# Performance work log

Measured on AMD Instinct MI355X. Metric: run time of the kernel, lower is better.

The kernel has to match this reference:

```python
import jax, jax.numpy as jnp
from jax import lax
import numpy as np

D_MODEL = 2048
NUM_EXPERTS = 16
NUM_TOKENS = 8192  # must be divisible by NUM_EXPERTS (balanced assignment)


def setup_inputs() -> dict:
    key = jax.random.key(0)
    k1, k2 = jax.random.split(key)
    features = jax.random.normal(k1, (NUM_TOKENS, D_MODEL), dtype=jnp.float32)
    # gate weight (orthogonal init in torch; gaussian is fine for a numerical baseline)
    W = jax.random.normal(k2, (NUM_EXPERTS, D_MODEL), dtype=jnp.float32) * 0.1
    b = jnp.zeros((NUM_EXPERTS,), dtype=jnp.float32)
    return {"features": features, "W": W, "b": b, "is_training": 1}


def _balanced_assignment(scores):
    """Greedy balanced assignment: each expert receives exactly T//E tokens.
    Deterministic stand-in for the cpp auction-based balanced_assignment: scan
    over tokens, each token takes its best-scoring expert with remaining capacity.
    Returns sort_by_expert: token indices sorted (stably) by assigned expert."""
    T, E = scores.shape
    cap_per_expert = T // E

    def step(cap, s):  # cap: [E] remaining capacity, s: [E] token's scores
        masked = jnp.where(cap > 0, s, -jnp.inf)
        e = jnp.argmax(masked)
        return cap.at[e].add(-1), e

    _, tok2exp = lax.scan(step, jnp.full((E,), cap_per_expert, dtype=jnp.int32), scores)
    sort_by_expert = jnp.argsort(tok2exp, stable=True)  # [T] token ids grouped by expert
    return sort_by_expert


def reference(features, W, b, is_training):
    # gating computed under no_grad in the original
    affinities = lax.stop_gradient(features @ W.T + b)  # [T, E]
    T, E = affinities.shape
    cap = T // E

    sort_by_expert = _balanced_assignment(affinities)

    routing_probs = jax.nn.softmax(affinities, axis=1)  # [T, E]

    # gather_scores: permute probs into expert order, pick each token's score for
    # its assigned expert, then un-permute back to original token order.
    sorted_probs = routing_probs[sort_by_expert]                 # [T, E]
    expert_idx = (jnp.arange(T) // cap)[:, None]                 # [T, 1], balanced splits
    gathered = jnp.take_along_axis(sorted_probs, expert_idx, axis=1)  # [T, 1]
    i_sort = jnp.argsort(sort_by_expert)                         # inverse permutation
    gathered_scores = gathered[i_sort]                           # [T, 1]

    return sort_by_expert, gathered_scores
```

## Files before the change

### kernel.cpp

```cpp
#include <hip/hip_runtime.h>
#include <hip/hip_bf16.h>
#include <math.h>

#define T_TOK 8192
#define D_MODEL 2048
#define N_EXP 16
#define CAP 512
#define NSEG (T_TOK / 64)


__device__ __forceinline__ unsigned int f2ord(float f) {
    unsigned int b = __float_as_uint(f);
    return (b & 0x80000000u) ? ~b : (b | 0x80000000u);
}

__global__ __launch_bounds__(512, 4) void gemm_finalize_kernel(
    const float* __restrict__ feat, const float* __restrict__ W,
    const float* __restrict__ bias,
    unsigned long long* __restrict__ pref, float* __restrict__ probs)
{
    __shared__ float flds[8][D_MODEL];
    __shared__ float afft[8][N_EXP];

    const int tid  = threadIdx.x;
    const int wave = tid >> 6, lane = tid & 63;
    const int tbase = blockIdx.x * 8;

    {
        const float4* src = (const float4*)(feat + (size_t)tbase * D_MODEL);
        float4* dst = (float4*)&flds[0][0];
        #pragma unroll
        for (int i = 0; i < 8; ++i)
            dst[tid + i * 512] = src[tid + i * 512];
    }

    const float* w0 = W + (size_t)(wave * 2) * D_MODEL + lane * 4;
    const float* w1 = w0 + D_MODEL;

    float acc[16];
    #pragma unroll
    for (int i = 0; i < 16; ++i) acc[i] = 0.f;

    float4 wv0 = *(const float4*)(w0);
    float4 wv1 = *(const float4*)(w1);
    __syncthreads();

    #pragma unroll
    for (int j = 0; j < 8; ++j) {
        float4 wn0, wn1;
        if (j < 7) {
            wn0 = *(const float4*)(w0 + (j + 1) * 256);
            wn1 = *(const float4*)(w1 + (j + 1) * 256);
        } else {
            wn0 = wv0; wn1 = wv1;
        }
        const float* fl = &flds[0][0] + j * 256 + lane * 4;
        #pragma unroll
        for (int r = 0; r < 8; ++r) {
            float4 f = *(const float4*)(fl + r * D_MODEL);
            acc[r * 2 + 0] += f.x * wv0.x;
            acc[r * 2 + 0] += f.y * wv0.y;
            acc[r * 2 + 0] += f.z * wv0.z;
            acc[r * 2 + 0] += f.w * wv0.w;
            acc[r * 2 + 1] += f.x * wv1.x;
            acc[r * 2 + 1] += f.y * wv1.y;
            acc[r * 2 + 1] += f.z * wv1.z;
            acc[r * 2 + 1] += f.w * wv1.w;
        }
        wv0 = wn0; wv1 = wn1;
    }

    #pragma unroll
    for (int step = 0; step < 4; ++step) {
        const int m    = 1 << step;
        const int half = 8 >> step;
        const bool hi  = (lane & m) != 0;
        #pragma unroll
        for (int jj = 0; jj < half; ++jj) {
            float send = hi ? acc[jj] : acc[jj + half];
            float recv = __shfl_xor(send, m, 64);
            acc[jj] = (hi ? acc[jj + half] : acc[jj]) + recv;
        }
    }
    acc[0] += __shfl_xor(acc[0], 16, 64);
    acc[0] += __shfl_xor(acc[0], 32, 64);

    if (lane < 16) {
        const int slot = ((lane & 1) << 3) | (((lane >> 1) & 1) << 2)
                       | (((lane >> 2) & 1) << 1) | ((lane >> 3) & 1);
        const int r = slot >> 1, el = slot & 1;
        afft[r][wave * 2 + el] = acc[0];
    }
    __syncthreads();

    const int tk = tbase + wave;
    const int j  = lane & 15;
    float v = afft[wave][j] + bias[j];

    float mx = v;
    #pragma unroll
    for (int d = 1; d < 16; d <<= 1)
        mx = fmaxf(mx, __shfl_xor(mx, d, 16));

    float ex = __expf(v - mx);

    float s = 0.f;
    #pragma unroll
    for (int e2 = 0; e2 < N_EXP; ++e2)
        s += __shfl(ex, e2, 16);

    if (lane < 16)
        probs[(size_t)tk * N_EXP + lane] = ex / s;

    unsigned long long key = ((unsigned long long)f2ord(v) << 4)
                           | (unsigned long long)(15 - j);
    int rank = 0;
    #pragma unroll
    for (int d = 1; d < 16; ++d) {
        unsigned long long o = __shfl_xor(key, d, 16);
        rank += (o > key) ? 1 : 0;
    }
    unsigned long long contrib = ((unsigned long long)j) << (4 * (15 - rank));
    #pragma unroll
    for (int d = 1; d < 16; d <<= 1)
        contrib |= __shfl_xor(contrib, d, 16);
    if (lane == 0)
        pref[tk] = contrib;
}

__global__ __launch_bounds__(512, 1) void events_kernel(
    const unsigned long long* __restrict__ pref, int* __restrict__ evt,
    int* __restrict__ gsync)
{
    __shared__ unsigned long long segmask[N_EXP][NSEG];
    __shared__ int fparr[N_EXP];

    const int tid  = threadIdx.x;
    const int wave = tid >> 6, lane = tid & 63;
    const unsigned long long lt_mask = (1ull << lane) - 1ull;

    if (tid == 0) *gsync = 0;

    unsigned long long myPref[16];
    #pragma unroll
    for (int k = 0; k < 16; ++k) myPref[k] = pref[tid + 512 * k];

    #pragma unroll
    for (int k = 0; k < 16; ++k) {
        const int s = k * 8 + wave;
        const int c = (int)(myPref[k] >> 60);
        #pragma unroll
        for (int e = 0; e < N_EXP; ++e) {
            unsigned long long mm = __ballot(c == e);
            if (lane == e) segmask[e][s] = mm;
        }
    }
    __syncthreads();

    const int eA = wave, eB = wave + 8;
    int capA = CAP, capB = CAP;
    unsigned long long m0A = 0, m1A = 0, m0B = 0, m1B = 0;
    int excl0A = 0, excl1A = 0, excl0B = 0, excl1B = 0;
    int segF = 0;
    unsigned long long mlep = 0;
    unsigned int avail = 0xFFFFu;
    int myp = 0, myf = 0;

    for (int round = 0; round < N_EXP; ++round) {
        {
            int exf = (segF < 64) ? __shfl(excl0A, segF, 64) : __shfl(excl1A, segF - 64, 64);
            unsigned long long mf = (segF < 64) ? __shfl(m0A, segF, 64) : __shfl(m1A, segF - 64, 64);
            capA -= exf + (int)__popcll(mf & mlep);
            exf = (segF < 64) ? __shfl(excl0B, segF, 64) : __shfl(excl1B, segF - 64, 64);
            mf  = (segF < 64) ? __shfl(m0B, segF, 64) : __shfl(m1B, segF - 64, 64);
            capB -= exf + (int)__popcll(mf & mlep);
        }

        unsigned long long a0 = segmask[eA][lane];
        unsigned long long a1 = segmask[eA][64 + lane];
        unsigned long long b0 = segmask[eB][lane];
        unsigned long long b1 = segmask[eB][64 + lane];
        if (lane < segF)            { a0 = 0; b0 = 0; }
        else if (lane == segF)      { a0 &= ~mlep; b0 &= ~mlep; }
        if (64 + lane < segF)       { a1 = 0; b1 = 0; }
        else if (64 + lane == segF) { a1 &= ~mlep; b1 &= ~mlep; }
        m0A = a0; m1A = a1; m0B = b0; m1B = b1;

        const int c0A = (int)__popcll(a0), c1A = (int)__popcll(a1);
        const int c0B = (int)__popcll(b0), c1B = (int)__popcll(b1);
        int v0A = c0A, v1A = c1A, v0B = c0B, v1B = c1B;
        #pragma unroll
        for (int d = 1; d < 64; d <<= 1) {
            int t0 = __shfl_up(v0A, d, 64);
            int t1 = __shfl_up(v1A, d, 64);
            int t2 = __shfl_up(v0B, d, 64);
            int t3 = __shfl_up(v1B, d, 64);
            if (lane >= d) { v0A += t0; v1A += t1; v0B += t2; v1B += t3; }
        }
        const int tot0A = __shfl(v0A, 63, 64);
        const int tot0B = __shfl(v0B, 63, 64);
        excl0A = v0A - c0A;
        excl1A = tot0A + v1A - c1A;
        excl0B = v0B - c0B;
        excl1B = tot0B + v1B - c1B;

        int fpA = 0x7FFFFFFF;
        if ((avail >> eA) & 1u) {
            const int need = capA;
            int segc = -1, kk = 0;
            if (excl0A < need && excl0A + c0A >= need)      { segc = lane;      kk = need - excl0A; }
            else if (excl1A < need && excl1A + c1A >= need) { segc = 64 + lane; kk = need - excl1A; }
            unsigned long long bb = __ballot(segc >= 0);
            if (bb) {
                int l2    = __builtin_ctzll(bb);
                int sstar = __shfl(segc, l2, 64);
                int k2    = __shfl(kk,   l2, 64);
                unsigned long long msel = (sstar < 64) ? __shfl(a0, sstar, 64)
                                                       : __shfl(a1, sstar - 64, 64);
                int rr = (int)__popcll(msel & lt_mask);
                bool hit = ((msel >> lane) & 1ull) && (rr == k2 - 1);
                unsigned long long hb = __ballot(hit);
                fpA = sstar * 64 + __builtin_ctzll(hb);
            }
        }
        int fpB = 0x7FFFFFFF;
        if ((avail >> eB) & 1u) {
            const int need = capB;
            int segc = -1, kk = 0;
            if (excl0B < need && excl0B + c0B >= need)      { segc = lane;      kk = need - excl0B; }
            else if (excl1B < need && excl1B + c1B >= need) { segc = 64 + lane; kk = need - excl1B; }
            unsigned long long bb = __ballot(segc >= 0);
            if (bb) {
                int l2    = __builtin_ctzll(bb);
                int sstar = __shfl(segc, l2, 64);
                int k2    = __shfl(kk,   l2, 64);
                unsigned long long msel = (sstar < 64) ? __shfl(b0, sstar, 64)
                                                       : __shfl(b1, sstar - 64, 64);
                int rr = (int)__popcll(msel & lt_mask);
                bool hit = ((msel >> lane) & 1ull) && (rr == k2 - 1);
                unsigned long long hb = __ballot(hit);
                fpB = sstar * 64 + __builtin_ctzll(hb);
            }
        }
        if (lane == 0) { fparr[eA] = fpA; fparr[eB] = fpB; }
        __syncthreads();

        int pmin = 0x7FFFFFFF, fe = 0;
        #pragma unroll
        for (int e = 0; e < N_EXP; ++e) {
            int f = fparr[e];
            if (f < pmin) { pmin = f; fe = e; }
        }
        if (tid == round) { myp = pmin; myf = fe; }

        const int nsegF = pmin >> 6;
        const unsigned long long nmlep = ((pmin & 63) == 63) ? ~0ull
                                         : ((1ull << ((pmin & 63) + 1)) - 1ull);
        const unsigned int navail = avail & ~(1u << fe);

        if (round < N_EXP - 1) {
            #pragma unroll
            for (int k = 0; k < 16; ++k) {
                const int s = k * 8 + wave;
                if (s >= nsegF) {
                    unsigned long long m = segmask[fe][s];
                    if (s == nsegF) m &= ~nmlep;
                    if ((m >> lane) & 1ull) {
                        unsigned long long pp = myPref[k];
                        int e2 = (int)(pp >> 60);
                        while (!((navail >> e2) & 1u)) { pp <<= 4; e2 = (int)(pp >> 60); }
                        atomicOr(&segmask[e2][s], 1ull << lane);
                    }
                }
            }
        }
        segF = nsegF; mlep = nmlep; avail = navail;
        __syncthreads();
    }

    if (tid < N_EXP) { evt[tid] = myp; evt[N_EXP + tid] = myf; }
}

__global__ __launch_bounds__(256) void choice_write_kernel(
    const unsigned long long* __restrict__ pref, const int* __restrict__ evt,
    const float* __restrict__ probs, int* __restrict__ bcnt, int* __restrict__ gsync,
    float* __restrict__ out0, float* __restrict__ out1)
{
    __shared__ int evp[N_EXP], evf[N_EXP];
    __shared__ int sc[4][N_EXP];
    __shared__ int base[N_EXP];
    const int tid = threadIdx.x, b = blockIdx.x;
    const int wave = tid >> 6, lane = tid & 63;
    const unsigned long long lt_mask = (1ull << lane) - 1ull;

    if (tid < N_EXP) evp[tid] = evt[tid];
    else if (tid < 2 * N_EXP) evf[tid - N_EXP] = evt[tid];
    __syncthreads();

    const int t = b * 256 + tid;
    unsigned int mask = 0xFFFFu;
    #pragma unroll
    for (int jj = 0; jj < N_EXP; ++jj)
        if (evp[jj] < t) mask &= ~(1u << evf[jj]);

    unsigned long long pp = pref[t];
    int e = (int)(pp >> 60);
    while (!((mask >> e) & 1u)) { pp <<= 4; e = (int)(pp >> 60); }

    unsigned long long own = 0ull;
    #pragma unroll
    for (int e2 = 0; e2 < N_EXP; ++e2) {
        unsigned long long mm = __ballot(e == e2);
        if (e == e2) own = mm;
        if (lane == e2) sc[wave][e2] = (int)__popcll(mm);
    }
    __syncthreads();

    if (tid < N_EXP)
        atomicExch(&bcnt[b * N_EXP + tid],
                   sc[0][tid] + sc[1][tid] + sc[2][tid] + sc[3][tid]);
    __syncthreads();

    if (tid == 0) {
        __threadfence();
        atomicAdd(gsync, 1);
        while (atomicAdd(gsync, 0) < 32) { __builtin_amdgcn_s_sleep(2); }
    }
    __syncthreads();

    if (tid < N_EXP) {
        int s = 0;
        for (int b2 = 0; b2 < b; ++b2) s += atomicAdd(&bcnt[b2 * N_EXP + tid], 0);
        base[tid] = s;
    }
    __syncthreads();

    int rank = (int)__popcll(own & lt_mask);
    for (int w2 = 0; w2 < wave; ++w2) rank += sc[w2][e];
    const int pos = base[e] + rank;
    out0[e * CAP + pos] = (float)t;
    out1[t] = probs[(size_t)t * N_EXP + e];
}

extern "C" void kernel_launch(void* const* d_in, const int* in_sizes, int n_in,
                              void* d_out, int out_size, void* d_ws, size_t ws_size,
                              hipStream_t stream) {
    const float* feat = (const float*)d_in[0];
    const float* W    = (const float*)d_in[1];
    const float* bias = (const float*)d_in[2];

    float* out = (float*)d_out;
    char*  ws  = (char*)d_ws;

    unsigned long long* pref = (unsigned long long*)(ws + 524288);
    float* probs             = (float*)(ws + 589824);
    int* evt                 = (int*)(ws + 1114112);
    int* gsync               = (int*)(ws + 1114240);
    int* bcnt                = (int*)(ws + 1122432);

    hipLaunchKernelGGL(gemm_finalize_kernel, dim3(T_TOK / 8), dim3(512), 0, stream,
                       feat, W, bias, pref, probs);
    hipLaunchKernelGGL(events_kernel, dim3(1), dim3(512), 0, stream,
                       pref, evt, gsync);
    hipLaunchKernelGGL(choice_write_kernel, dim3(T_TOK / 256), dim3(256), 0, stream,
                       pref, evt, probs, bcnt, gsync, out, out + T_TOK);
}
```

Baseline: 182.5 us.

## Fuse events and choice-write kernels with grid barrier; use global_load_lds for features

```diff
diff --git a/kernel.cpp b/kernel.cpp
--- a/kernel.cpp
+++ b/kernel.cpp
@@ -14,10 +14,16 @@
     return (b & 0x80000000u) ? ~b : (b | 0x80000000u);
 }
 
-__global__ __launch_bounds__(512, 4) void gemm_finalize_kernel(
+#define GLOBAL_LOAD_LDS16(g, l)                                            \
+    __builtin_amdgcn_global_load_lds(                                      \
+        (const __attribute__((address_space(1))) unsigned int*)(g),        \
+        (__attribute__((address_space(3))) unsigned int*)(l), 16, 0, 0)
+
+__global__ __launch_bounds__(512) void gemm_finalize_kernel(
     const float* __restrict__ feat, const float* __restrict__ W,
     const float* __restrict__ bias,
-    unsigned long long* __restrict__ pref, float* __restrict__ probs)
+    unsigned long long* __restrict__ pref, float* __restrict__ probs,
+    int* __restrict__ gsync)
 {
     __shared__ float flds[8][D_MODEL];
     __shared__ float afft[8][N_EXP];
@@ -26,12 +32,15 @@
     const int wave = tid >> 6, lane = tid & 63;
     const int tbase = blockIdx.x * 8;
 
+    if (blockIdx.x == 0 && tid == 0) { gsync[0] = 0; gsync[1] = 0; }
+
     {
-        const float4* src = (const float4*)(feat + (size_t)tbase * D_MODEL);
-        float4* dst = (float4*)&flds[0][0];
-        #pragma unroll
-        for (int i = 0; i < 8; ++i)
-            dst[tid + i * 512] = src[tid + i * 512];
+        const float* src = feat + (size_t)tbase * D_MODEL;
+        #pragma unroll
+        for (int i = 0; i < 8; ++i) {
+            const int idx = tid + i * 512;
+            GLOBAL_LOAD_LDS16(src + (size_t)idx * 4, &flds[0][0] + (size_t)idx * 4);
+        }
     }
 
     const float* w0 = W + (size_t)(wave * 2) * D_MODEL + lane * 4;
@@ -128,176 +137,180 @@
         pref[tk] = contrib;
 }
 
-__global__ __launch_bounds__(512, 1) void events_kernel(
-    const unsigned long long* __restrict__ pref, int* __restrict__ evt,
-    int* __restrict__ gsync)
+__global__ __launch_bounds__(512, 1) void events_choice_write_kernel(
+    const unsigned long long* __restrict__ pref, const float* __restrict__ probs,
+    int* __restrict__ evt, int* __restrict__ gsync, int* __restrict__ bcnt,
+    float* __restrict__ out0, float* __restrict__ out1)
 {
     __shared__ unsigned long long segmask[N_EXP][NSEG];
     __shared__ int fparr[N_EXP];
+    __shared__ int evp[N_EXP], evf[N_EXP];
+    __shared__ int sc[8][N_EXP];
+    __shared__ int base[N_EXP];
 
     const int tid  = threadIdx.x;
     const int wave = tid >> 6, lane = tid & 63;
     const unsigned long long lt_mask = (1ull << lane) - 1ull;
-
-    if (tid == 0) *gsync = 0;
-
-    unsigned long long myPref[16];
-    #pragma unroll
-    for (int k = 0; k < 16; ++k) myPref[k] = pref[tid + 512 * k];
-
-    #pragma unroll
-    for (int k = 0; k < 16; ++k) {
-        const int s = k * 8 + wave;
-        const int c = (int)(myPref[k] >> 60);
-        #pragma unroll
-        for (int e = 0; e < N_EXP; ++e) {
-            unsigned long long mm = __ballot(c == e);
-            if (lane == e) segmask[e][s] = mm;
-        }
-    }
-    __syncthreads();
-
-    const int eA = wave, eB = wave + 8;
-    int capA = CAP, capB = CAP;
-    unsigned long long m0A = 0, m1A = 0, m0B = 0, m1B = 0;
-    int excl0A = 0, excl1A = 0, excl0B = 0, excl1B = 0;
-    int segF = 0;
-    unsigned long long mlep = 0;
-    unsigned int avail = 0xFFFFu;
-    int myp = 0, myf = 0;
-
-    for (int round = 0; round < N_EXP; ++round) {
-        {
-            int exf = (segF < 64) ? __shfl(excl0A, segF, 64) : __shfl(excl1A, segF - 64, 64);
-            unsigned long long mf = (segF < 64) ? __shfl(m0A, segF, 64) : __shfl(m1A, segF - 64, 64);
-            capA -= exf + (int)__popcll(mf & mlep);
-            exf = (segF < 64) ? __shfl(excl0B, segF, 64) : __shfl(excl1B, segF - 64, 64);
-            mf  = (segF < 64) ? __shfl(m0B, segF, 64) : __shfl(m1B, segF - 64, 64);
-            capB -= exf + (int)__popcll(mf & mlep);
-        }
-
-        unsigned long long a0 = segmask[eA][lane];
-        unsigned long long a1 = segmask[eA][64 + lane];
-        unsigned long long b0 = segmask[eB][lane];
-        unsigned long long b1 = segmask[eB][64 + lane];
-        if (lane < segF)            { a0 = 0; b0 = 0; }
-        else if (lane == segF)      { a0 &= ~mlep; b0 &= ~mlep; }
-        if (64 + lane < segF)       { a1 = 0; b1 = 0; }
-        else if (64 + lane == segF) { a1 &= ~mlep; b1 &= ~mlep; }
-        m0A = a0; m1A = a1; m0B = b0; m1B = b1;
-
-        const int c0A = (int)__popcll(a0), c1A = (int)__popcll(a1);
-        const int c0B = (int)__popcll(b0), c1B = (int)__popcll(b1);
-        int v0A = c0A, v1A = c1A, v0B = c0B, v1B = c1B;
-        #pragma unroll
-        for (int d = 1; d < 64; d <<= 1) {
-            int t0 = __shfl_up(v0A, d, 64);
-            int t1 = __shfl_up(v1A, d, 64);
-            int t2 = __shfl_up(v0B, d, 64);
-            int t3 = __shfl_up(v1B, d, 64);
-            if (lane >= d) { v0A += t0; v1A += t1; v0B += t2; v1B += t3; }
-        }
-        const int tot0A = __shfl(v0A, 63, 64);
-        const int tot0B = __shfl(v0B, 63, 64);
-        excl0A = v0A - c0A;
-        excl1A = tot0A + v1A - c1A;
-        excl0B = v0B - c0B;
-        excl1B = tot0B + v1B - c1B;
-
-        int fpA = 0x7FFFFFFF;
-        if ((avail >> eA) & 1u) {
-            const int need = capA;
-            int segc = -1, kk = 0;
-            if (excl0A < need && excl0A + c0A >= need)      { segc = lane;      kk = need - excl0A; }
-            else if (excl1A < need && excl1A + c1A >= need) { segc = 64 + lane; kk = need - excl1A; }
-            unsigned long long bb = __ballot(segc >= 0);
-            if (bb) {
-                int l2    = __builtin_ctzll(bb);
-                int sstar = __shfl(segc, l2, 64);
-                int k2    = __shfl(kk,   l2, 64);
-                unsigned long long msel = (sstar < 64) ? __shfl(a0, sstar, 64)
-                                                       : __shfl(a1, sstar - 64, 64);
-                int rr = (int)__popcll(msel & lt_mask);
-                bool hit = ((msel >> lane) & 1ull) && (rr == k2 - 1);
-                unsigned long long hb = __ballot(hit);
-                fpA = sstar * 64 + __builtin_ctzll(hb);
-            }
-        }
-        int fpB = 0x7FFFFFFF;
-        if ((avail >> eB) & 1u) {
-            const int need = capB;
-            int segc = -1, kk = 0;
-            if (excl0B < need && excl0B + c0B >= need)      { segc = lane;      kk = need - excl0B; }
-            else if (excl1B < need && excl1B + c1B >= need) { segc = 64 + lane; kk = need - excl1B; }
-            unsigned long long bb = __ballot(segc >= 0);
-            if (bb) {
-                int l2    = __builtin_ctzll(bb);
-                int sstar = __shfl(segc, l2, 64);
-                int k2    = __shfl(kk,   l2, 64);
-                unsigned long long msel = (sstar < 64) ? __shfl(b0, sstar, 64)
-                                                       : __shfl(b1, sstar - 64, 64);
-                int rr = (int)__popcll(msel & lt_mask);
-                bool hit = ((msel >> lane) & 1ull) && (rr == k2 - 1);
-                unsigned long long hb = __ballot(hit);
-                fpB = sstar * 64 + __builtin_ctzll(hb);
-            }
-        }
-        if (lane == 0) { fparr[eA] = fpA; fparr[eB] = fpB; }
+    const int b = blockIdx.x;
+
+    if (b == 0) {
+        unsigned long long myPref[16];
+        #pragma unroll
+        for (int k = 0; k < 16; ++k) myPref[k] = pref[tid + 512 * k];
+
+        #pragma unroll
+        for (int k = 0; k < 16; ++k) {
+            const int s = k * 8 + wave;
+            const int c = (int)(myPref[k] >> 60);
+            #pragma unroll
+            for (int e = 0; e < N_EXP; ++e) {
+                unsigned long long mm = __ballot(c == e);
+                if (lane == e) segmask[e][s] = mm;
+            }
+        }
         __syncthreads();
 
-        int pmin = 0x7FFFFFFF, fe = 0;
-        #pragma unroll
-        for (int e = 0; e < N_EXP; ++e) {
-            int f = fparr[e];
-            if (f < pmin) { pmin = f; fe = e; }
-        }
-        if (tid == round) { myp = pmin; myf = fe; }
-
-        const int nsegF = pmin >> 6;
-        const unsigned long long nmlep = ((pmin & 63) == 63) ? ~0ull
-                                         : ((1ull << ((pmin & 63) + 1)) - 1ull);
-        const unsigned int navail = avail & ~(1u << fe);
-
-        if (round < N_EXP - 1) {
+        const int eA = wave, eB = wave + 8;
+        int capA = CAP, capB = CAP;
+        unsigned long long m0A = 0, m1A = 0, m0B = 0, m1B = 0;
+        int excl0A = 0, excl1A = 0, excl0B = 0, excl1B = 0;
+        int segF = 0;
+        unsigned long long mlep = 0;
+        unsigned int avail = 0xFFFFu;
+        int myp = 0, myf = 0;
+
+        for (int round = 0; round < N_EXP; ++round) {
+            {
+                int exf = (segF < 64) ? __shfl(excl0A, segF, 64) : __shfl(excl1A, segF - 64, 64);
+                unsigned long long mf = (segF < 64) ? __shfl(m0A, segF, 64) : __shfl(m1A, segF - 64, 64);
+                capA -= exf + (int)__popcll(mf & mlep);
+                exf = (segF < 64) ? __shfl(excl0B, segF, 64) : __shfl(excl1B, segF - 64, 64);
+                mf  = (segF < 64) ? __shfl(m0B, segF, 64) : __shfl(m1B, segF - 64, 64);
+                capB -= exf + (int)__popcll(mf & mlep);
+            }
+
+            unsigned long long a0 = segmask[eA][lane];
+            unsigned long long a1 = segmask[eA][64 + lane];
+            unsigned long long b0 = segmask[eB][lane];
+            unsigned long long b1 = segmask[eB][64 + lane];
+            if (lane < segF)            { a0 = 0; b0 = 0; }
+            else if (lane == segF)      { a0 &= ~mlep; b0 &= ~mlep; }
+            if (64 + lane < segF)       { a1 = 0; b1 = 0; }
+            else if (64 + lane == segF) { a1 &= ~mlep; b1 &= ~mlep; }
+            m0A = a0; m1A = a1; m0B = b0; m1B = b1;
+
+            const int c0A = (int)__popcll(a0), c1A = (int)__popcll(a1);
+            const int c0B = (int)__popcll(b0), c1B = (int)__popcll(b1);
+            int v0A = c0A, v1A = c1A, v0B = c0B, v1B = c1B;
             #pragma unroll
-            for (int k = 0; k < 16; ++k) {
-                const int s = k * 8 + wave;
-                if (s >= nsegF) {
-                    unsigned long long m = segmask[fe][s];
-                    if (s == nsegF) m &= ~nmlep;
-                    if ((m >> lane) & 1ull) {
-                        unsigned long long pp = myPref[k];
-                        int e2 = (int)(pp >> 60);
-                        while (!((navail >> e2) & 1u)) { pp <<= 4; e2 = (int)(pp >> 60); }
-                        atomicOr(&segmask[e2][s], 1ull << lane);
+            for (int d = 1; d < 64; d <<= 1) {
+                int t0 = __shfl_up(v0A, d, 64);
+                int t1 = __shfl_up(v1A, d, 64);
+                int t2 = __shfl_up(v0B, d, 64);
+                int t3 = __shfl_up(v1B, d, 64);
+                if (lane >= d) { v0A += t0; v1A += t1; v0B += t2; v1B += t3; }
+            }
+            const int tot0A = __shfl(v0A, 63, 64);
+            const int tot0B = __shfl(v0B, 63, 64);
+            excl0A = v0A - c0A;
+            excl1A = tot0A + v1A - c1A;
+            excl0B = v0B - c0B;
+            excl1B = tot0B + v1B - c1B;
+
+            int fpA = 0x7FFFFFFF;
+            if ((avail >> eA) & 1u) {
+                const int need = capA;
+                int segc = -1, kk = 0;
+                if (excl0A < need && excl0A + c0A >= need)      { segc = lane;      kk = need - excl0A; }
+                else if (excl1A < need && excl1A + c1A >= need) { segc = 64 + lane; kk = need - excl1A; }
+                unsigned long long bb = __ballot(segc >= 0);
+                if (bb) {
+                    int l2    = __builtin_ctzll(bb);
+                    int sstar = __shfl(segc, l2, 64);
+                    int k2    = __shfl(kk,   l2, 64);
+                    unsigned long long msel = (sstar < 64) ? __shfl(a0, sstar, 64)
+                                                           : __shfl(a1, sstar - 64, 64);
+                    int rr = (int)__popcll(msel & lt_mask);
+                    bool hit = ((msel >> lane) & 1ull) && (rr == k2 - 1);
+                    unsigned long long hb = __ballot(hit);
+                    fpA = sstar * 64 + __builtin_ctzll(hb);
+                }
+            }
+            int fpB = 0x7FFFFFFF;
+            if ((avail >> eB) & 1u) {
+                const int need = capB;
+                int segc = -1, kk = 0;
+                if (excl0B < need && excl0B + c0B >= need)      { segc = lane;      kk = need - excl0B; }
+                else if (excl1B < need && excl1B + c1B >= need) { segc = 64 + lane; kk = need - excl1B; }
+                unsigned long long bb = __ballot(segc >= 0);
+                if (bb) {
+                    int l2    = __builtin_ctzll(bb);
+                    int sstar = __shfl(segc, l2, 64);
+                    int k2    = __shfl(kk,   l2, 64);
+                    unsigned long long msel = (sstar < 64) ? __shfl(b0, sstar, 64)
+                                                           : __shfl(b1, sstar - 64, 64);
+                    int rr = (int)__popcll(msel & lt_mask);
+                    bool hit = ((msel >> lane) & 1ull) && (rr == k2 - 1);
+                    unsigned long long hb = __ballot(hit);
+                    fpB = sstar * 64 + __builtin_ctzll(hb);
+                }
+            }
+            if (lane == 0) { fparr[eA] = fpA; fparr[eB] = fpB; }
+            __syncthreads();
+
+            int pmin = 0x7FFFFFFF, fe = 0;
+            #pragma unroll
+            for (int e = 0; e < N_EXP; ++e) {
+                int f = fparr[e];
+                if (f < pmin) { pmin = f; fe = e; }
+            }
+            if (tid == round) { myp = pmin; myf = fe; }
+
+            const int nsegF = pmin >> 6;
+            const unsigned long long nmlep = ((pmin & 63) == 63) ? ~0ull
+                                             : ((1ull << ((pmin & 63) + 1)) - 1ull);
+            const unsigned int navail = avail & ~(1u << fe);
+
+            if (round < N_EXP - 1) {
+                #pragma unroll
+                for (int k = 0; k < 16; ++k) {
+                    const int s = k * 8 + wave;
+                    if (s >= nsegF) {
+                        unsigned long long m = segmask[fe][s];
+                        if (s == nsegF) m &= ~nmlep;
+                        if ((m >> lane) & 1ull) {
+                            unsigned long long pp = myPref[k];
+                            int e2 = (int)(pp >> 60);
+                            while (!((navail >> e2) & 1u)) { pp <<= 4; e2 = (int)(pp >> 60); }
+                            atomicOr(&segmask[e2][s], 1ull << lane);
+                        }
                     }
                 }
             }
-        }
-        segF = nsegF; mlep = nmlep; avail = navail;
-        __syncthreads();
-    }
-
-    if (tid < N_EXP) { evt[tid] = myp; evt[N_EXP + tid] = myf; }
-}
-
-__global__ __launch_bounds__(256) void choice_write_kernel(
-    const unsigned long long* __restrict__ pref, const int* __restrict__ evt,
-    const float* __restrict__ probs, int* __restrict__ bcnt, int* __restrict__ gsync,
-    float* __restrict__ out0, float* __restrict__ out1)
-{
-    __shared__ int evp[N_EXP], evf[N_EXP];
-    __shared__ int sc[4][N_EXP];
-    __shared__ int base[N_EXP];
-    const int tid = threadIdx.x, b = blockIdx.x;
-    const int wave = tid >> 6, lane = tid & 63;
-    const unsigned long long lt_mask = (1ull << lane) - 1ull;
-
-    if (tid < N_EXP) evp[tid] = evt[tid];
-    else if (tid < 2 * N_EXP) evf[tid - N_EXP] = evt[tid];
-    __syncthreads();
-
-    const int t = b * 256 + tid;
+            segF = nsegF; mlep = nmlep; avail = navail;
+            __syncthreads();
+        }
+
+        if (tid < N_EXP) {
+            atomicExch(&evt[tid], myp);
+            atomicExch(&evt[N_EXP + tid], myf);
+        }
+    }
+
+    __syncthreads();
+    if (tid == 0) {
+        __threadfence();
+        atomicAdd(&gsync[0], 1);
+        while (atomicAdd(&gsync[0], 0) < 16) { __builtin_amdgcn_s_sleep(2); }
+        __threadfence();
+    }
+    __syncthreads();
+
+    if (tid < N_EXP) evp[tid] = atomicAdd(&evt[tid], 0);
+    else if (tid < 2 * N_EXP) evf[tid - N_EXP] = atomicAdd(&evt[tid], 0);
+    __syncthreads();
+
+    const int t = b * 512 + tid;
     unsigned int mask = 0xFFFFu;
     #pragma unroll
     for (int jj = 0; jj < N_EXP; ++jj)
@@ -316,15 +329,19 @@
     }
     __syncthreads();
 
-    if (tid < N_EXP)
-        atomicExch(&bcnt[b * N_EXP + tid],
-                   sc[0][tid] + sc[1][tid] + sc[2][tid] + sc[3][tid]);
-    __syncthreads();
-
+    if (tid < N_EXP) {
+        int s = 0;
+        #pragma unroll
+        for (int w2 = 0; w2 < 8; ++w2) s += sc[w2][tid];
+        atomicExch(&bcnt[b * N_EXP + tid], s);
+    }
+
+    __syncthreads();
     if (tid == 0) {
         __threadfence();
-        atomicAdd(gsync, 1);
-        while (atomicAdd(gsync, 0) < 32) { __builtin_amdgcn_s_sleep(2); }
+        atomicAdd(&gsync[1], 1);
+        while (atomicAdd(&gsync[1], 0) < 16) { __builtin_amdgcn_s_sleep(2); }
+        __threadfence();
     }
     __syncthreads();
 
@@ -359,9 +376,7 @@
     int* bcnt                = (int*)(ws + 1122432);
 
     hipLaunchKernelGGL(gemm_finalize_kernel, dim3(T_TOK / 8), dim3(512), 0, stream,
-                       feat, W, bias, pref, probs);
-    hipLaunchKernelGGL(events_kernel, dim3(1), dim3(512), 0, stream,
-                       pref, evt, gsync);
-    hipLaunchKernelGGL(choice_write_kernel, dim3(T_TOK / 256), dim3(256), 0, stream,
-                       pref, evt, probs, bcnt, gsync, out, out + T_TOK);
+                       feat, W, bias, pref, probs, gsync);
+    hipLaunchKernelGGL(events_choice_write_kernel, dim3(16), dim3(512), 0, stream,
+                       pref, probs, evt, gsync, bcnt, out, out + T_TOK);
 }
```

New measurement: 175.4 us. 1.04x faster.
